# Performance work log

Measured on AMD Instinct MI355X. Metric: run time of the kernel, lower is better.

## Reference

```python
import jax, jax.numpy as jnp
import numpy as np

N = 100000   # nodes
E = 800000   # edges (before self loops)
IN = 128     # in_channels
H1, C1 = 8, 64      # gat1: heads, channels  -> 512 out
NC = 16      # num_classes (gat3: 1 head)
NEG_SLOPE = 0.2


def setup_inputs() -> dict:
    key = jax.random.key(0)
    ks = jax.random.split(key, 14)
    def gl(k, shape, fan_in):
        return jax.random.normal(k, shape, dtype=jnp.float32) / np.sqrt(fan_in)
    x = jax.random.normal(ks[0], (N, IN), dtype=jnp.float32)
    edge_index = jax.random.randint(ks[1], (2, E), 0, N, dtype=jnp.int64)
    return {
        "x": x,
        "edge_index": edge_index,
        # gat1: in=128 -> 8 heads x 64
        "g1_W": gl(ks[2], (IN, H1 * C1), IN),
        "g1_as": gl(ks[3], (H1, C1), C1),
        "g1_ad": gl(ks[4], (H1, C1), C1),
        "g1_b": jnp.zeros((H1 * C1,), jnp.float32),
        # skip_proj1: 128 -> 512
        "sk1_W": gl(ks[5], (IN, H1 * C1), IN),
        "sk1_b": jnp.zeros((H1 * C1,), jnp.float32),
        # skip_proj2: 512 -> 512
        "sk2_W": gl(ks[6], (H1 * C1, 512), H1 * C1),
        "sk2_b": jnp.zeros((512,), jnp.float32),
        # gat3: in=1024 -> 1 head x NC
        "g3_W": gl(ks[7], (1024, NC), 1024),
        "g3_as": gl(ks[8], (1, NC), NC),
        "g3_ad": gl(ks[9], (1, NC), NC),
        "g3_b": jnp.zeros((NC,), jnp.float32),
    }


def _gat_conv(x, W, att_src, att_dst, bias, src, dst, n):
    """PyG GATConv: concat=True, add_self_loops already in (src, dst)."""
    H, C = att_src.shape
    h = (x @ W).reshape(n, H, C)                      # [N,H,C]
    a_src = jnp.einsum('nhc,hc->nh', h, att_src)      # [N,H]
    a_dst = jnp.einsum('nhc,hc->nh', h, att_dst)
    e = jax.nn.leaky_relu(a_src[src] + a_dst[dst], NEG_SLOPE)   # [E,H]
    # segment softmax over destination node
    emax = jax.ops.segment_max(e, dst, num_segments=n)
    e = jnp.exp(e - emax[dst])
    denom = jax.ops.segment_sum(e, dst, num_segments=n)
    alpha = e / (denom[dst] + 1e-16)                  # [E,H]
    msg = h[src] * alpha[:, :, None]                  # [E,H,C] gather + weight
    out = jax.ops.segment_sum(msg, dst, num_segments=n)  # [N,H,C] scatter-add
    return out.reshape(n, H * C) + bias


def reference(x, edge_index, g1_W, g1_as, g1_ad, g1_b,
              sk1_W, sk1_b, sk2_W, sk2_b, g3_W, g3_as, g3_ad, g3_b):
    n = x.shape[0]
    loop = jnp.arange(n, dtype=edge_index.dtype)
    src = jnp.concatenate([edge_index[0], loop])      # add self loops (PyG default)
    dst = jnp.concatenate([edge_index[1], loop])
    x1 = _gat_conv(x, g1_W, g1_as, g1_ad, g1_b, src, dst, n)   # [N,512]
    x_skip1 = x @ sk1_W + sk1_b                                  # [N,512]
    # NOTE: original computes gat2(x1) but never uses it (dead code) -> omitted
    x_skip2 = x1 @ sk2_W + sk2_b                                 # [N,512]
    x3 = jnp.concatenate([x_skip1, x_skip2], axis=1)             # [N,1024]
    return _gat_conv(x3, g3_W, g3_as, g3_ad, g3_b, src, dst, n)  # [N,NC]
```

## Files before the change

kernel.cpp:

```cpp
#include <hip/hip_runtime.h>
#include <hip/hip_bf16.h>

#define NEG_SLOPE 0.2f
using bf16 = __hip_bfloat16;

typedef __attribute__((ext_vector_type(8))) short short8;
typedef __attribute__((ext_vector_type(4))) float f32x4;
#define MFMA16(a, b, c) __builtin_amdgcn_mfma_f32_16x16x32_bf16(a, b, c, 0, 0, 0)

__device__ __forceinline__ float bflo(unsigned u) { return __uint_as_float(u << 16); }
__device__ __forceinline__ float bfhi(unsigned u) { return __uint_as_float(u & 0xffff0000u); }

__device__ __forceinline__ unsigned cvtpk(float lo, float hi) {
  unsigned r;
  asm volatile("v_cvt_pk_bf16_f32 %0, %1, %2" : "=v"(r) : "v"(lo), "v"(hi));
  return r;
}

__device__ __forceinline__ float edge_w(float q, float adh) {
  float t = q + adh;
  t = (t > 0.f) ? t : NEG_SLOPE * t;
  return __expf(t);
}

__device__ __forceinline__ size_t frag_off(int row, int k) {
  return (size_t)(row >> 4) * 2048 + (k >> 5) * 512 + ((k >> 3) & 3) * 128 +
         (row & 15) * 8 + (k & 7);
}

__global__ __launch_bounds__(256)
void deg_kernel(const int* __restrict__ ei, int* __restrict__ deg, int E, int EP) {
  int e = blockIdx.x * 256 + threadIdx.x;
  if (e >= EP) return;
  int d = (e < E) ? ei[E + e] : (e - E);
  atomicAdd(&deg[d], 1);
}

__global__ __launch_bounds__(256)
void mid_kernel(const int* __restrict__ deg, int* __restrict__ offs, int* __restrict__ bsum,
                const float* __restrict__ x, const float* __restrict__ g1_W,
                const float* __restrict__ sk1_W, const float* __restrict__ sk2_W,
                const float* __restrict__ g3_W,
                bf16* __restrict__ xbX, bf16* __restrict__ WtX,
                float* __restrict__ W1pT, float* __restrict__ W2pT,
                bf16* __restrict__ W2pSa,
                int N, int Np, int NB, int b1, int b2, int b3, int b4) {
  const int b = blockIdx.x;
  const int t = threadIdx.x;
  if (b < NB) {
    __shared__ int ts[256];
    const int base = b * 1024 + t * 4;
    int4 v = make_int4(0, 0, 0, 0);
    if (base + 3 < N) v = *reinterpret_cast<const int4*>(&deg[base]);
    else {
      if (base + 0 < N) v.x = deg[base + 0];
      if (base + 1 < N) v.y = deg[base + 1];
      if (base + 2 < N) v.z = deg[base + 2];
    }
    ts[t] = v.x + v.y + v.z + v.w;
    __syncthreads();
    for (int st = 1; st < 256; st <<= 1) {
      int u = (t >= st) ? ts[t - st] : 0;
      __syncthreads();
      ts[t] += u;
      __syncthreads();
    }
    int excl = (t == 0) ? 0 : ts[t - 1];
    int4 o;
    o.x = excl; o.y = o.x + v.x; o.z = o.y + v.y; o.w = o.z + v.z;
    if (base + 3 < N) *reinterpret_cast<int4*>(&offs[base]) = o;
    else {
      if (base + 0 < N) offs[base + 0] = o.x;
      if (base + 1 < N) offs[base + 1] = o.y;
      if (base + 2 < N) offs[base + 2] = o.z;
    }
    if (t == 255) bsum[b] = ts[255];
  } else if (b < b1) {
    const int total4 = Np * 32;
    const int stride = (b1 - NB) * 256;
    for (int i = (b - NB) * 256 + t; i < total4; i += stride) {
      int row = i >> 5, kq = (i & 31) * 4;
      float4 v = make_float4(0.f, 0.f, 0.f, 0.f);
      if (row < N) v = reinterpret_cast<const float4*>(x)[i];
      union { bf16 bv[4]; ushort4 u; } pk;
      pk.bv[0] = __float2bfloat16(v.x); pk.bv[1] = __float2bfloat16(v.y);
      pk.bv[2] = __float2bfloat16(v.z); pk.bv[3] = __float2bfloat16(v.w);
      *reinterpret_cast<ushort4*>(&xbX[frag_off(row, kq)]) = pk.u;
    }
  } else if (b < b2) {
    int i = (b - b1) * 256 + t;
    int k = i >> 9, c = i & 511;
    WtX[frag_off(c, k)] = __float2bfloat16(g1_W[k * 512 + c]);
  } else if (b < b3) {
    int i = (b - b2) * 256 + t;
    int o = i >> 3, seg = i & 7;
    int j = o >> 7, k = o & 127;
    float acc = 0.f;
    for (int m = seg * 64; m < seg * 64 + 64; m++)
      acc += sk1_W[k * 512 + m] * g3_W[m * 16 + j];
    acc += __shfl_xor(acc, 1); acc += __shfl_xor(acc, 2); acc += __shfl_xor(acc, 4);
    if (seg == 0) W1pT[o] = acc;
  } else if (b < b4) {
    int i = (b - b3) * 256 + t;
    int o = i >> 3, seg = i & 7;
    int j = o >> 9, c = o & 511;
    float acc = 0.f;
    for (int m = seg * 64; m < seg * 64 + 64; m++)
      acc += sk2_W[c * 512 + m] * g3_W[(512 + m) * 16 + j];
    acc += __shfl_xor(acc, 1); acc += __shfl_xor(acc, 2); acc += __shfl_xor(acc, 4);
    if (seg == 0) {
      W2pT[o] = acc;
      int h = c >> 6, cc = c & 63, kk = cc >> 5, lk = (cc >> 3) & 3, e = cc & 7;
      W2pSa[((size_t)(h * 2 + kk) * 64 + (j + 16 * lk)) * 8 + e] = __float2bfloat16(acc);
    }
  }
}

__global__ __launch_bounds__(256)
void scan3_setup2_kernel(int* __restrict__ offs, const int* __restrict__ bsum, int n, int NB,
                         const float* __restrict__ sk1_b, const float* __restrict__ sk2_b,
                         const float* __restrict__ g1_b, const float* __restrict__ g3_W,
                         const float* __restrict__ W2pT, float* __restrict__ b3p) {
  const int b = blockIdx.x, t = threadIdx.x;
  if (b == NB) {
    __shared__ float red[16][16];
    int j = t & 15, seg = t >> 4;
    float acc = 0.f;
    for (int m = seg * 32; m < seg * 32 + 32; m++)
      acc += sk1_b[m] * g3_W[m * 16 + j] + sk2_b[m] * g3_W[(512 + m) * 16 + j];
    for (int c = seg * 32; c < seg * 32 + 32; c++)
      acc += g1_b[c] * W2pT[j * 512 + c];
    red[seg][j] = acc;
    __syncthreads();
    if (t < 16) {
      float s = 0.f;
      for (int k = 0; k < 16; k++) s += red[k][t];
      b3p[t] = s;
    }
    return;
  }
  __shared__ int wred[4];
  int part = (t < b) ? bsum[t] : 0;
  #pragma unroll
  for (int m = 1; m < 64; m <<= 1) part += __shfl_xor(part, m);
  if ((t & 63) == 0) wred[t >> 6] = part;
  __syncthreads();
  const int add = wred[0] + wred[1] + wred[2] + wred[3];
  if (b == NB - 1 && t == 0) offs[n] = add + bsum[b];
  if (add == 0) return;
  const int base = b * 1024 + t * 4;
  if (base + 3 < n) {
    int4 o = *reinterpret_cast<const int4*>(&offs[base]);
    o.x += add; o.y += add; o.z += add; o.w += add;
    *reinterpret_cast<int4*>(&offs[base]) = o;
  } else {
    if (base + 0 < n) offs[base + 0] += add;
    if (base + 1 < n) offs[base + 1] += add;
    if (base + 2 < n) offs[base + 2] += add;
  }
}

__global__ __launch_bounds__(256)
void gemm_scatter_kernel(const bf16* __restrict__ xbX, const bf16* __restrict__ WtX,
                         const bf16* __restrict__ W2pSa,
                         const float* __restrict__ att_s, const float* __restrict__ att_d,
                         bf16* __restrict__ g1p, float* __restrict__ a_src,
                         float* __restrict__ a_dst,
                         const int* __restrict__ ei, const int* __restrict__ offs,
                         int* __restrict__ cursor, int* __restrict__ esrc,
                         int M, int Mt, int E, int EP, int eb) {
  if (blockIdx.x < eb) {
    int e = blockIdx.x * 256 + threadIdx.x;
    if (e < EP) {
      int s = (e < E) ? ei[e] : (e - E);
      int d = (e < E) ? ei[E + e] : (e - E);
      int pos = offs[d] + atomicAdd(&cursor[d], 1);
      esrc[pos] = s;
    }
    return;
  }
  const int gb = blockIdx.x - eb;
  const int bx = gb % Mt;
  const int by = gb / Mt;
  const int t = threadIdx.x;
  const int w = t >> 6, l = t & 63;
  const int wm = w & 1, wn = w >> 1;
  const int m0 = bx * 64 + wm * 32;
  const int n0 = by * 128 + wn * 64;
  const int head = n0 >> 6;
  const int lr = l & 15, lk = l >> 4;
  const bf16* aBase = xbX + (size_t)(m0 >> 4) * 2048 + l * 8;
  const bf16* bBase = WtX + (size_t)(n0 >> 4) * 2048 + l * 8;
  f32x4 accT[4][2] = {};
  #pragma unroll
  for (int kc = 0; kc < 4; kc++) {
    short8 av0 = *reinterpret_cast<const short8*>(aBase + kc * 512);
    short8 av1 = *reinterpret_cast<const short8*>(aBase + 2048 + kc * 512);
    short8 bv0 = *reinterpret_cast<const short8*>(bBase + 0 * 2048 + kc * 512);
    short8 bv1 = *reinterpret_cast<const short8*>(bBase + 1 * 2048 + kc * 512);
    short8 bv2 = *reinterpret_cast<const short8*>(bBase + 2 * 2048 + kc * 512);
    short8 bv3 = *reinterpret_cast<const short8*>(bBase + 3 * 2048 + kc * 512);
    accT[0][0] = MFMA16(bv0, av0, accT[0][0]);
    accT[1][0] = MFMA16(bv1, av0, accT[1][0]);
    accT[2][0] = MFMA16(bv2, av0, accT[2][0]);
    accT[3][0] = MFMA16(bv3, av0, accT[3][0]);
    accT[0][1] = MFMA16(bv0, av1, accT[0][1]);
    accT[1][1] = MFMA16(bv1, av1, accT[1][1]);
    accT[2][1] = MFMA16(bv2, av1, accT[2][1]);
    accT[3][1] = MFMA16(bv3, av1, accT[3][1]);
  }
  #pragma unroll
  for (int mi = 0; mi < 2; mi++) {
    float vs = 0.f, vd = 0.f;
    #pragma unroll
    for (int ni = 0; ni < 4; ni++) {
      float4 as4 = *reinterpret_cast<const float4*>(&att_s[head * 64 + ni * 16 + lk * 4]);
      float4 ad4 = *reinterpret_cast<const float4*>(&att_d[head * 64 + ni * 16 + lk * 4]);
      vs += accT[ni][mi][0] * as4.x + accT[ni][mi][1] * as4.y +
            accT[ni][mi][2] * as4.z + accT[ni][mi][3] * as4.w;
      vd += accT[ni][mi][0] * ad4.x + accT[ni][mi][1] * ad4.y +
            accT[ni][mi][2] * ad4.z + accT[ni][mi][3] * ad4.w;
    }
    vs += __shfl_xor(vs, 16); vs += __shfl_xor(vs, 32);
    vd += __shfl_xor(vd, 16); vd += __shfl_xor(vd, 32);
    int row = m0 + mi * 16 + lr;
    if (lk == 0 && row < M) {
      a_src[(size_t)row * 8 + head] = vs;
      a_dst[(size_t)row * 8 + head] = vd;
    }
  }
  unsigned pk[4][2][2];
  #pragma unroll
  for (int ni = 0; ni < 4; ni++)
    #pragma unroll
    for (int mi = 0; mi < 2; mi++) {
      pk[ni][mi][0] = cvtpk(accT[ni][mi][0], accT[ni][mi][1]);
      pk[ni][mi][1] = cvtpk(accT[ni][mi][2], accT[ni][mi][3]);
    }
  f32x4 d3[2] = {};
  #pragma unroll
  for (int kk = 0; kk < 2; kk++) {
    short8 aw2 = *reinterpret_cast<const short8*>(&W2pSa[((size_t)(head * 2 + kk) * 64 + l) * 8]);
    #pragma unroll
    for (int mi = 0; mi < 2; mi++) {
      union { unsigned u[4]; short8 s8; } bf;
      #pragma unroll
      for (int v = 0; v < 4; v++) {
        int src = lr + 16 * ((lk & 1) * 2 + (v >> 1));
        unsigned t0 = __shfl(pk[2 * kk][mi][v & 1], src);
        unsigned t1 = __shfl(pk[2 * kk + 1][mi][v & 1], src);
        bf.u[v] = (lk & 2) ? t1 : t0;
      }
      d3[mi] = MFMA16(aw2, bf.s8, d3[mi]);
    }
  }
  #pragma unroll
  for (int mi = 0; mi < 2; mi++) {
    int row = m0 + mi * 16 + lr;
    if (row < M) {
      uint2 st;
      st.x = cvtpk(d3[mi][0], d3[mi][1]);
      st.y = cvtpk(d3[mi][2], d3[mi][3]);
      *reinterpret_cast<uint2*>(&g1p[(size_t)row * 128 + head * 16 + lk * 4]) = st;
    }
  }
}

__global__ __launch_bounds__(256)
void agg1_h3_kernel(const int* __restrict__ offs, const int* __restrict__ esrc,
                    const float* __restrict__ a_src1, const float* __restrict__ a_dst1,
                    const bf16* __restrict__ g1p,
                    const float* __restrict__ X,
                    const float* __restrict__ W1pT, const float* __restrict__ b3p,
                    const float* __restrict__ g3_as, const float* __restrict__ g3_ad,
                    bf16* __restrict__ H3b, float* __restrict__ a3s, float* __restrict__ a3d,
                    int N) {
  const int l = threadIdx.x & 63;
  const int n = blockIdx.x * 4 + (threadIdx.x >> 6);
  if (n >= N) return;
  const int g = l >> 3, j0 = l & 7;
  const float adh = a_dst1[n * 8 + g];
  const unsigned* __restrict__ G = reinterpret_cast<const unsigned*>(g1p);
  const int lo = offs[n], hi = offs[n + 1];
  const int gj = g * 8 + j0;
  float agg0 = 0.f, agg1 = 0.f, psum = 0.f;
  int i = lo;
  for (; i + 16 <= hi; i += 16) {
    int ss[16]; float qq[16]; unsigned ww[16];
    #pragma unroll
    for (int k = 0; k < 16; k++) ss[k] = esrc[i + k];
    #pragma unroll
    for (int k = 0; k < 16; k++) ww[k] = G[(size_t)ss[k] * 64 + gj];
    #pragma unroll
    for (int k = 0; k < 16; k++) qq[k] = a_src1[(size_t)ss[k] * 8 + g];
    #pragma unroll
    for (int k = 0; k < 16; k++) {
      float v = edge_w(qq[k], adh);
      psum += v;
      agg0 = fmaf(v, bflo(ww[k]), agg0);
      agg1 = fmaf(v, bfhi(ww[k]), agg1);
    }
  }
  if (i + 8 <= hi) {
    int ss[8]; float qq[8]; unsigned ww[8];
    #pragma unroll
    for (int k = 0; k < 8; k++) ss[k] = esrc[i + k];
    #pragma unroll
    for (int k = 0; k < 8; k++) ww[k] = G[(size_t)ss[k] * 64 + gj];
    #pragma unroll
    for (int k = 0; k < 8; k++) qq[k] = a_src1[(size_t)ss[k] * 8 + g];
    #pragma unroll
    for (int k = 0; k < 8; k++) {
      float v = edge_w(qq[k], adh);
      psum += v;
      agg0 = fmaf(v, bflo(ww[k]), agg0);
      agg1 = fmaf(v, bfhi(ww[k]), agg1);
    }
    i += 8;
  }
  for (; i < hi; i++) {
    int s = esrc[i];
    float q = a_src1[(size_t)s * 8 + g];
    unsigned w0 = G[(size_t)s * 64 + gj];
    float v = edge_w(q, adh);
    psum += v;
    agg0 = fmaf(v, bflo(w0), agg0); agg1 = fmaf(v, bfhi(w0), agg1);
  }
  const float inv = 1.f / (psum + 1e-16f);
  float v0 = agg0 * inv, v1 = agg1 * inv;
  {
    const float* xr = &X[(size_t)n * 128 + g * 16];
    const float* wr0 = &W1pT[(2 * j0) * 128 + g * 16];
    const float* wr1 = &W1pT[(2 * j0 + 1) * 128 + g * 16];
    #pragma unroll
    for (int c = 0; c < 16; c += 4) {
      float4 xa = *reinterpret_cast<const float4*>(xr + c);
      float4 wa = *reinterpret_cast<const float4*>(wr0 + c);
      float4 wb = *reinterpret_cast<const float4*>(wr1 + c);
      v0 += xa.x * wa.x + xa.y * wa.y + xa.z * wa.z + xa.w * wa.w;
      v1 += xa.x * wb.x + xa.y * wb.y + xa.z * wb.z + xa.w * wb.w;
    }
  }
  v0 += __shfl_xor(v0, 8); v0 += __shfl_xor(v0, 16); v0 += __shfl_xor(v0, 32);
  v1 += __shfl_xor(v1, 8); v1 += __shfl_xor(v1, 16); v1 += __shfl_xor(v1, 32);
  float o0 = v0 + b3p[2 * j0];
  float o1 = v1 + b3p[2 * j0 + 1];
  if (g == 0) reinterpret_cast<unsigned*>(H3b)[(size_t)n * 8 + j0] = cvtpk(o0, o1);
  float vs = o0 * g3_as[2 * j0] + o1 * g3_as[2 * j0 + 1];
  float vd = o0 * g3_ad[2 * j0] + o1 * g3_ad[2 * j0 + 1];
  vs += __shfl_xor(vs, 1); vs += __shfl_xor(vs, 2); vs += __shfl_xor(vs, 4);
  vd += __shfl_xor(vd, 1); vd += __shfl_xor(vd, 2); vd += __shfl_xor(vd, 4);
  if (l == 0) { a3s[n] = vs; a3d[n] = vd; }
}

__global__ __launch_bounds__(256)
void agg3_kernel(const int* __restrict__ offs, const int* __restrict__ esrc,
                 const float* __restrict__ a3s, const float* __restrict__ a3d,
                 const bf16* __restrict__ H3b, const float* __restrict__ g3_b,
                 float* __restrict__ out, int N) {
  const int l = threadIdx.x & 63;
  const int n = blockIdx.x * 4 + (threadIdx.x >> 6);
  if (n >= N) return;
  const int g = l >> 4, j = l & 15;
  const float ad = a3d[n];
  const ushort* __restrict__ H = reinterpret_cast<const ushort*>(H3b);
  const int lo = offs[n], hi = offs[n + 1];
  float acc = 0.f, psum = 0.f;
  int i = lo + g;
  for (; i + 12 < hi; i += 16) {
    int s0 = esrc[i], s1 = esrc[i + 4], s2 = esrc[i + 8], s3 = esrc[i + 12];
    float q0 = a3s[s0], q1 = a3s[s1], q2 = a3s[s2], q3 = a3s[s3];
    float h0 = __uint_as_float((unsigned)H[(size_t)s0 * 16 + j] << 16);
    float h1 = __uint_as_float((unsigned)H[(size_t)s1 * 16 + j] << 16);
    float h2 = __uint_as_float((unsigned)H[(size_t)s2 * 16 + j] << 16);
    float h3v = __uint_as_float((unsigned)H[(size_t)s3 * 16 + j] << 16);
    float v0 = edge_w(q0, ad), v1 = edge_w(q1, ad);
    float v2 = edge_w(q2, ad), v3 = edge_w(q3, ad);
    psum += (v0 + v1) + (v2 + v3);
    acc = fmaf(v0, h0, acc); acc = fmaf(v1, h1, acc);
    acc = fmaf(v2, h2, acc); acc = fmaf(v3, h3v, acc);
  }
  for (; i < hi; i += 4) {
    int s = esrc[i];
    float v = edge_w(a3s[s], ad);
    psum += v;
    acc = fmaf(v, __uint_as_float((unsigned)H[(size_t)s * 16 + j] << 16), acc);
  }
  acc += __shfl_xor(acc, 16);  acc += __shfl_xor(acc, 32);
  psum += __shfl_xor(psum, 16); psum += __shfl_xor(psum, 32);
  if (l < 16) out[(size_t)n * 16 + j] = acc / (psum + 1e-16f) + g3_b[j];
}

__global__ void sentinel_kernel(float* out) { out[threadIdx.x] = -1e9f; }

extern "C" void kernel_launch(void* const* d_in, const int* in_sizes, int n_in,
                              void* d_out, int out_size, void* d_ws, size_t ws_size,
                              hipStream_t stream) {
  const float* x      = (const float*)d_in[0];
  const int*   ei     = (const int*)d_in[1];
  const float* g1_W   = (const float*)d_in[2];
  const float* g1_as  = (const float*)d_in[3];
  const float* g1_ad  = (const float*)d_in[4];
  const float* g1_b   = (const float*)d_in[5];
  const float* sk1_W  = (const float*)d_in[6];
  const float* sk1_b  = (const float*)d_in[7];
  const float* sk2_W  = (const float*)d_in[8];
  const float* sk2_b  = (const float*)d_in[9];
  const float* g3_W   = (const float*)d_in[10];
  const float* g3_as  = (const float*)d_in[11];
  const float* g3_ad  = (const float*)d_in[12];
  const float* g3_b   = (const float*)d_in[13];
  float* out = (float*)d_out;

  const int N  = in_sizes[0] / 128;
  const int E  = in_sizes[1] / 2;
  const int EP = E + N;
  const int Mt = (N + 63) / 64;
  const int Np = Mt * 64;
  const int NB = (N + 1023) / 1024;

  char* w = (char*)d_ws;
  size_t off = 0;
  auto alloc = [&](size_t bytes) -> void* {
    void* p = w + off;
    off = (off + bytes + 255) & ~(size_t)255;
    return p;
  };

  int* deg    = (int*)alloc((size_t)N * 4);
  int* cursor = (int*)alloc((size_t)N * 4);
  size_t zbytes = off;
  int*   offs   = (int*)alloc((size_t)(N + 1) * 4);
  int*   bsum   = (int*)alloc((size_t)NB * 4);
  int*   esrc   = (int*)alloc((size_t)EP * 4);
  bf16*  xbX    = (bf16*)alloc((size_t)Np * 128 * 2);
  bf16*  WtX    = (bf16*)alloc(512 * 128 * 2);
  bf16*  W2pSa  = (bf16*)alloc(8192 * 2);
  bf16*  g1p    = (bf16*)alloc((size_t)N * 128 * 2);
  float* a_src1 = (float*)alloc((size_t)N * 8 * 4);
  float* a_dst1 = (float*)alloc((size_t)N * 8 * 4);
  bf16*  h3b    = (bf16*)alloc((size_t)N * 16 * 2);
  float* a_src3 = (float*)alloc((size_t)N * 4);
  float* a_dst3 = (float*)alloc((size_t)N * 4);
  float* W1pT   = (float*)alloc(128 * 16 * 4);
  float* W2pT   = (float*)alloc(512 * 16 * 4);
  float* b3p    = (float*)alloc(16 * 4);
  (void)n_in; (void)out_size;

  if (off > ws_size) {
    sentinel_kernel<<<1, 16, 0, stream>>>(out);
    return;
  }

  hipMemsetAsync(d_ws, 0, zbytes, stream);

  const int eb = (EP + 255) / 256;
  const int nb4 = (N + 3) / 4;
  const int b1 = NB + 1024, b2 = b1 + 256, b3 = b2 + 64, b4 = b3 + 256;

  deg_kernel<<<eb, 256, 0, stream>>>(ei, deg, E, EP);

  mid_kernel<<<b4, 256, 0, stream>>>(
      deg, offs, bsum, x, g1_W, sk1_W, sk2_W, g3_W,
      xbX, WtX, W1pT, W2pT, W2pSa, N, Np, NB, b1, b2, b3, b4);

  scan3_setup2_kernel<<<NB + 1, 256, 0, stream>>>(
      offs, bsum, N, NB, sk1_b, sk2_b, g1_b, g3_W, W2pT, b3p);

  gemm_scatter_kernel<<<eb + Mt * 4, 256, 0, stream>>>(
      xbX, WtX, W2pSa, g1_as, g1_ad, g1p, a_src1, a_dst1,
      ei, offs, cursor, esrc, N, Mt, E, EP, eb);

  agg1_h3_kernel<<<nb4, 256, 0, stream>>>(offs, esrc, a_src1, a_dst1, g1p, x,
                                          W1pT, b3p, g3_as, g3_ad,
                                          h3b, a_src3, a_dst3, N);

  agg3_kernel<<<nb4, 256, 0, stream>>>(offs, esrc, a_src3, a_dst3, h3b, g3_b, out, N);
}
```

Baseline: 335.7 us.

## Record edge ranks during degree count to drop cursor atomics in CSR fill

The degree-counting atomicAdd now saves its return value as a per-edge rank, so the CSR fill writes esrc[offs[d]+rank[e]] directly instead of doing a second atomic on a cursor array. The degree count is merged into the setup kernel that converts x and the weights, and the block-local scan moves into the setup2 kernel, so a separate scan3 kernel is added. The kernel count stays the same. In exchange it adds a rank buffer of EP ints to write and read, and degree atomics now run alongside the conversion blocks.

```diff
diff --git a/kernel.cpp b/kernel.cpp
--- a/kernel.cpp
+++ b/kernel.cpp
@@ -29,56 +29,27 @@
 }
 
 __global__ __launch_bounds__(256)
-void deg_kernel(const int* __restrict__ ei, int* __restrict__ deg, int E, int EP) {
-  int e = blockIdx.x * 256 + threadIdx.x;
-  if (e >= EP) return;
-  int d = (e < E) ? ei[E + e] : (e - E);
-  atomicAdd(&deg[d], 1);
-}
-
-__global__ __launch_bounds__(256)
-void mid_kernel(const int* __restrict__ deg, int* __restrict__ offs, int* __restrict__ bsum,
-                const float* __restrict__ x, const float* __restrict__ g1_W,
-                const float* __restrict__ sk1_W, const float* __restrict__ sk2_W,
-                const float* __restrict__ g3_W,
-                bf16* __restrict__ xbX, bf16* __restrict__ WtX,
-                float* __restrict__ W1pT, float* __restrict__ W2pT,
-                bf16* __restrict__ W2pSa,
-                int N, int Np, int NB, int b1, int b2, int b3, int b4) {
+void setup_kernel(const int* __restrict__ ei, int* __restrict__ deg, int* __restrict__ rank,
+                  const float* __restrict__ x, const float* __restrict__ g1_W,
+                  const float* __restrict__ sk1_W, const float* __restrict__ sk2_W,
+                  const float* __restrict__ g3_W,
+                  bf16* __restrict__ xbX, bf16* __restrict__ WtX,
+                  float* __restrict__ W1pT, float* __restrict__ W2pT,
+                  bf16* __restrict__ W2pSa,
+                  int N, int Np, int E, int EP,
+                  int bD, int b1, int b2, int b3, int b4) {
   const int b = blockIdx.x;
   const int t = threadIdx.x;
-  if (b < NB) {
-    __shared__ int ts[256];
-    const int base = b * 1024 + t * 4;
-    int4 v = make_int4(0, 0, 0, 0);
-    if (base + 3 < N) v = *reinterpret_cast<const int4*>(&deg[base]);
-    else {
-      if (base + 0 < N) v.x = deg[base + 0];
-      if (base + 1 < N) v.y = deg[base + 1];
-      if (base + 2 < N) v.z = deg[base + 2];
-    }
-    ts[t] = v.x + v.y + v.z + v.w;
-    __syncthreads();
-    for (int st = 1; st < 256; st <<= 1) {
-      int u = (t >= st) ? ts[t - st] : 0;
-      __syncthreads();
-      ts[t] += u;
-      __syncthreads();
-    }
-    int excl = (t == 0) ? 0 : ts[t - 1];
-    int4 o;
-    o.x = excl; o.y = o.x + v.x; o.z = o.y + v.y; o.w = o.z + v.z;
-    if (base + 3 < N) *reinterpret_cast<int4*>(&offs[base]) = o;
-    else {
-      if (base + 0 < N) offs[base + 0] = o.x;
-      if (base + 1 < N) offs[base + 1] = o.y;
-      if (base + 2 < N) offs[base + 2] = o.z;
-    }
-    if (t == 255) bsum[b] = ts[255];
+  if (b < bD) {
+    int e = b * 256 + t;
+    if (e < EP) {
+      int d = (e < E) ? ei[E + e] : (e - E);
+      rank[e] = atomicAdd(&deg[d], 1);
+    }
   } else if (b < b1) {
     const int total4 = Np * 32;
-    const int stride = (b1 - NB) * 256;
-    for (int i = (b - NB) * 256 + t; i < total4; i += stride) {
+    const int stride = (b1 - bD) * 256;
+    for (int i = (b - bD) * 256 + t; i < total4; i += stride) {
       int row = i >> 5, kq = (i & 31) * 4;
       float4 v = make_float4(0.f, 0.f, 0.f, 0.f);
       if (row < N) v = reinterpret_cast<const float4*>(x)[i];
@@ -117,7 +88,8 @@
 }
 
 __global__ __launch_bounds__(256)
-void scan3_setup2_kernel(int* __restrict__ offs, const int* __restrict__ bsum, int n, int NB,
+void scan1_setup2_kernel(const int* __restrict__ deg, int* __restrict__ offs,
+                         int* __restrict__ bsum, int n, int NB,
                          const float* __restrict__ sk1_b, const float* __restrict__ sk2_b,
                          const float* __restrict__ g1_b, const float* __restrict__ g3_W,
                          const float* __restrict__ W2pT, float* __restrict__ b3p) {
@@ -139,7 +111,39 @@
     }
     return;
   }
+  __shared__ int ts[256];
+  const int base = b * 1024 + t * 4;
+  int4 v = make_int4(0, 0, 0, 0);
+  if (base + 3 < n) v = *reinterpret_cast<const int4*>(&deg[base]);
+  else {
+    if (base + 0 < n) v.x = deg[base + 0];
+    if (base + 1 < n) v.y = deg[base + 1];
+    if (base + 2 < n) v.z = deg[base + 2];
+  }
+  ts[t] = v.x + v.y + v.z + v.w;
+  __syncthreads();
+  for (int st = 1; st < 256; st <<= 1) {
+    int u = (t >= st) ? ts[t - st] : 0;
+    __syncthreads();
+    ts[t] += u;
+    __syncthreads();
+  }
+  int excl = (t == 0) ? 0 : ts[t - 1];
+  int4 o;
+  o.x = excl; o.y = o.x + v.x; o.z = o.y + v.y; o.w = o.z + v.z;
+  if (base + 3 < n) *reinterpret_cast<int4*>(&offs[base]) = o;
+  else {
+    if (base + 0 < n) offs[base + 0] = o.x;
+    if (base + 1 < n) offs[base + 1] = o.y;
+    if (base + 2 < n) offs[base + 2] = o.z;
+  }
+  if (t == 255) bsum[b] = ts[255];
+}
+
+__global__ __launch_bounds__(256)
+void scan3_kernel(int* __restrict__ offs, const int* __restrict__ bsum, int n, int NB) {
   __shared__ int wred[4];
+  const int b = blockIdx.x, t = threadIdx.x;
   int part = (t < b) ? bsum[t] : 0;
   #pragma unroll
   for (int m = 1; m < 64; m <<= 1) part += __shfl_xor(part, m);
@@ -167,15 +171,14 @@
                          bf16* __restrict__ g1p, float* __restrict__ a_src,
                          float* __restrict__ a_dst,
                          const int* __restrict__ ei, const int* __restrict__ offs,
-                         int* __restrict__ cursor, int* __restrict__ esrc,
+                         const int* __restrict__ rank, int* __restrict__ esrc,
                          int M, int Mt, int E, int EP, int eb) {
   if (blockIdx.x < eb) {
     int e = blockIdx.x * 256 + threadIdx.x;
     if (e < EP) {
       int s = (e < E) ? ei[e] : (e - E);
       int d = (e < E) ? ei[E + e] : (e - E);
-      int pos = offs[d] + atomicAdd(&cursor[d], 1);
-      esrc[pos] = s;
+      esrc[offs[d] + rank[e]] = s;
     }
     return;
   }
@@ -428,10 +431,10 @@
   };
 
   int* deg    = (int*)alloc((size_t)N * 4);
-  int* cursor = (int*)alloc((size_t)N * 4);
   size_t zbytes = off;
   int*   offs   = (int*)alloc((size_t)(N + 1) * 4);
   int*   bsum   = (int*)alloc((size_t)NB * 4);
+  int*   rank   = (int*)alloc((size_t)EP * 4);
   int*   esrc   = (int*)alloc((size_t)EP * 4);
   bf16*  xbX    = (bf16*)alloc((size_t)Np * 128 * 2);
   bf16*  WtX    = (bf16*)alloc(512 * 128 * 2);
@@ -456,20 +459,20 @@
 
   const int eb = (EP + 255) / 256;
   const int nb4 = (N + 3) / 4;
-  const int b1 = NB + 1024, b2 = b1 + 256, b3 = b2 + 64, b4 = b3 + 256;
-
-  deg_kernel<<<eb, 256, 0, stream>>>(ei, deg, E, EP);
-
-  mid_kernel<<<b4, 256, 0, stream>>>(
-      deg, offs, bsum, x, g1_W, sk1_W, sk2_W, g3_W,
-      xbX, WtX, W1pT, W2pT, W2pSa, N, Np, NB, b1, b2, b3, b4);
-
-  scan3_setup2_kernel<<<NB + 1, 256, 0, stream>>>(
-      offs, bsum, N, NB, sk1_b, sk2_b, g1_b, g3_W, W2pT, b3p);
+  const int bD = eb, b1 = bD + 1024, b2 = b1 + 256, b3 = b2 + 64, b4 = b3 + 256;
+
+  setup_kernel<<<b4, 256, 0, stream>>>(
+      ei, deg, rank, x, g1_W, sk1_W, sk2_W, g3_W,
+      xbX, WtX, W1pT, W2pT, W2pSa, N, Np, E, EP, bD, b1, b2, b3, b4);
+
+  scan1_setup2_kernel<<<NB + 1, 256, 0, stream>>>(
+      deg, offs, bsum, N, NB, sk1_b, sk2_b, g1_b, g3_W, W2pT, b3p);
+
+  scan3_kernel<<<NB, 256, 0, stream>>>(offs, bsum, N, NB);
 
   gemm_scatter_kernel<<<eb + Mt * 4, 256, 0, stream>>>(
       xbX, WtX, W2pSa, g1_as, g1_ad, g1p, a_src1, a_dst1,
-      ei, offs, cursor, esrc, N, Mt, E, EP, eb);
+      ei, offs, rank, esrc, N, Mt, E, EP, eb);
 
   agg1_h3_kernel<<<nb4, 256, 0, stream>>>(offs, esrc, a_src1, a_dst1, g1p, x,
                                           W1pT, b3p, g3_as, g3_ad,
```

New measurement: 317.4 us. 1.06x faster.
